# Performance work log

Hardware: AMD Instinct MI355X
Metric: run time of the kernel (lower is better)

The kernel has to match this reference:

```python
import jax, jax.numpy as jnp
import numpy as np

B, C, D, H, W = 2, 32, 16, 64, 64
SCALER = 8
CK = C // SCALER  # qk channels = 4


def setup_inputs() -> dict:
    key = jax.random.key(0)
    ks = jax.random.split(key, 8)
    s = 0.05
    return {
        "x": jax.random.normal(ks[0], (B, C, D, H, W), dtype=jnp.float32),
        "Wk": jax.random.normal(ks[1], (CK, C), dtype=jnp.float32) * s,
        "bk": jax.random.normal(ks[2], (CK,), dtype=jnp.float32) * s,
        "Wq": jax.random.normal(ks[3], (CK, C), dtype=jnp.float32) * s,
        "bq": jax.random.normal(ks[4], (CK,), dtype=jnp.float32) * s,
        "Wv": jax.random.normal(ks[5], (C, C), dtype=jnp.float32) * s,
        "bv": jax.random.normal(ks[6], (C,), dtype=jnp.float32) * s,
        "gamma": jnp.ones((1,), dtype=jnp.float32),
    }


def _proj(x, Wt, b):
    # 1x1x1 Conv3d == channel matmul: (o,c) x (b,c,d,h,w) -> (b,o,d,h,w)
    y = jnp.einsum('oc,bcdhw->bodhw', Wt, x) + b[None, :, None, None, None]
    return y


def reference(x, Wk, bk, Wq, bq, Wv, bv, gamma):
    b, c, d, h, w = x.shape
    hw = h * w
    xk = _proj(x, Wk, bk).reshape(b, -1, hw)   # (b, ck*d, hw)
    xq = _proj(x, Wq, bq).reshape(b, -1, hw)   # (b, ck*d, hw)
    xv = _proj(x, Wv, bv).reshape(b, -1, hw)   # (b, c*d,  hw)
    # dot[b,i,j] = sum_e xk[b,e,i] * xq[b,e,j]  -> (b, hw, hw)
    dot = jnp.einsum('bei,bej->bij', xk, xq)
    att = jax.nn.softmax(dot, axis=-1)          # softmax over last dim
    # x_a[b,m,i] = sum_j xv[b,m,j] * att[b,i,j]
    x_a = jnp.einsum('bmj,bij->bmi', xv, att)
    x_a = x_a.reshape(b, c, d, h, w)
    return gamma[0] * x + x_a
```

## Files before the change

kernel.cpp:

```cpp
#include <hip/hip_runtime.h>
#include <hip/hip_bf16.h>

#define B_   2
#define C_   32
#define D_   16
#define HW_  4096
#define CK_  4
#define E_   64
#define M_   512
#define JC_  4

typedef __attribute__((ext_vector_type(8)))  short bf16x8;
typedef __attribute__((ext_vector_type(16))) float f32x16;
typedef __attribute__((ext_vector_type(2)))  unsigned int u32x2;

union U4 { unsigned int u[4]; bf16x8 v; };

__device__ __forceinline__ short f2bf(float f) {
    __hip_bfloat16 h = __float2bfloat16(f);
    return *reinterpret_cast<short*>(&h);
}
__device__ __forceinline__ unsigned short f2bfu(float f) {
    __hip_bfloat16 h = __float2bfloat16(f);
    return *reinterpret_cast<unsigned short*>(&h);
}

__global__ void prep_kernel(
    const float* __restrict__ Wk, const float* __restrict__ bk,
    const float* __restrict__ Wq, const float* __restrict__ bq,
    const float* __restrict__ Wv, const float* __restrict__ bv,
    short* __restrict__ Wall, float* __restrict__ ball)
{
    int t = threadIdx.x;
    for (int i = t; i < 64*C_; i += 256) {
        int o = i >> 5, cc = i & 31;
        float val = (o < 32) ? Wv[o*C_ + cc]
                  : (o < 36) ? Wk[(o-32)*C_ + cc]
                  : (o < 40) ? Wq[(o-36)*C_ + cc] : 0.f;
        Wall[o*C_ + cc] = f2bf(val);
    }
    if (t < 64)
        ball[t] = (t < 32) ? bv[t] : (t < 36) ? bk[t-32] : (t < 40) ? bq[t-36] : 0.f;
}

__global__ __launch_bounds__(256) void proj_kernel(
    const float* __restrict__ x,
    const short* __restrict__ Wall, const float* __restrict__ ball,
    short* __restrict__ xk, short* __restrict__ xq,
    __hip_bfloat16* __restrict__ v)
{
    __shared__ short s_k[32*16], s_q[32*16];
    const int t    = threadIdx.x;
    const int lane = t & 63;
    const int w    = t >> 6;
    const int h    = lane >> 5;
    const int c    = lane & 31;

    const int pt = blockIdx.x & 127;
    const int dg = (blockIdx.x >> 7) & 3;
    const int b  = blockIdx.x >> 9;
    const int d  = dg*4 + w;
    const int p0 = pt*32;

    bf16x8 af[2][2];
    #pragma unroll
    for (int mt = 0; mt < 2; ++mt)
        #pragma unroll
        for (int s = 0; s < 2; ++s)
            af[mt][s] = *(const bf16x8*)(Wall + (mt*32 + c)*C_ + s*16 + h*8);

    U4 xb[2];
    #pragma unroll
    for (int s = 0; s < 2; ++s) {
        #pragma unroll
        for (int j = 0; j < 4; ++j) {
            int c0 = s*16 + h*8 + 2*j;
            union { float f; unsigned int u; } ua, ub;
            ua.f = x[(((size_t)(b*C_ + c0  )*D_ + d)*HW_) + p0 + c];
            ub.f = x[(((size_t)(b*C_ + c0+1)*D_ + d)*HW_) + p0 + c];
            xb[s].u[j] = __builtin_amdgcn_perm(ub.u, ua.u, 0x07060302);
        }
    }

    f32x16 a0, a1;
    #pragma unroll
    for (int r = 0; r < 16; ++r) { a0[r] = 0.f; a1[r] = 0.f; }
    #pragma unroll
    for (int s = 0; s < 2; ++s) {
        a0 = __builtin_amdgcn_mfma_f32_32x32x16_bf16(af[0][s], xb[s].v, a0, 0, 0, 0);
        a1 = __builtin_amdgcn_mfma_f32_32x32x16_bf16(af[1][s], xb[s].v, a1, 0, 0, 0);
    }

    #pragma unroll
    for (int r = 0; r < 16; ++r) {
        int o = (r & 3) + 8*(r >> 2) + 4*h;
        v[((size_t)b*M_ + (o*D_ + d))*HW_ + p0 + c] = __float2bfloat16(a0[r] + ball[o]);
    }

    #pragma unroll
    for (int r = 0; r < 4; ++r) {
        if (h == 0) s_k[c*16 + w*4 + r] = f2bf(a1[r] + ball[32 + r]);
        else        s_q[c*16 + w*4 + r] = f2bf(a1[r] + ball[36 + r]);
    }
    __syncthreads();

    const int p = t >> 3, seg = t & 7;
    size_t gb = ((size_t)b*HW_ + p0 + p)*E_ + dg*16 + seg*2;
    *(unsigned int*)(xk + gb) = *(const unsigned int*)(&s_k[p*16 + seg*2]);
    *(unsigned int*)(xq + gb) = *(const unsigned int*)(&s_q[p*16 + seg*2]);
}

__device__ __forceinline__ void load_lds16(const short* g, short* l) {
    __builtin_amdgcn_global_load_lds((const __attribute__((address_space(1))) void*)g,
                                     (__attribute__((address_space(3))) void*)l,
                                     16, 0, 0);
}

__global__ __launch_bounds__(256, 4) void attn_kernel(
    const short* __restrict__ xk_, const short* __restrict__ xq_,
    const short* __restrict__ v_,
    unsigned short* __restrict__ Op, float* __restrict__ lw)
{
    __shared__ short s_xq[2][2048];
    __shared__ short s_v [2][4096];

    const int t    = threadIdx.x;
    const int lane = t & 63;
    const int w    = t >> 6;
    const int h    = lane >> 5;
    const int c    = lane & 31;

    const int cls  = blockIdx.x & 7;
    const int b    = cls >> 2, mg = cls & 3;
    const int rest = blockIdx.x >> 3;
    const int ig   = rest & 31;
    const int jc   = rest >> 5;
    const int i0   = ig*128 + w*32;
    const int jbase = jc*(HW_/JC_);

    const short* xk_g = xk_ + (size_t)b*HW_*E_;
    const short* xq_g = xq_ + (size_t)b*HW_*E_;
    const short* v_g  = v_  + (size_t)b*M_*HW_ + (size_t)mg*128*HW_;

    bf16x8 kb[4];
    #pragma unroll
    for (int s = 0; s < 4; ++s)
        kb[s] = *(const bf16x8*)(xk_g + (size_t)(i0 + c)*E_ + s*16 + h*8);

    f32x16 acc[4];
    #pragma unroll
    for (int mt = 0; mt < 4; ++mt)
        #pragma unroll
        for (int r = 0; r < 16; ++r) acc[mt][r] = 0.f;
    float lp = 0.f;

    auto stage = [&](int buf, int j0) {
        {
            int r_ = w*8 + (lane>>3), cc = (lane&7) ^ (r_&7);
            load_lds16(xq_g + (size_t)(j0 + r_)*E_ + cc*8, &s_xq[buf][w*512]);
        }
        #pragma unroll
        for (int k = 0; k < 2; ++k) {
            int r0 = w*32 + k*16;
            int r_ = r0 + (lane>>2);
            int g  = (lane&3) ^ ((r_>>1)&3);
            load_lds16(v_g + (size_t)r_*HW_ + j0 + g*8, &s_v[buf][r0*32]);
        }
    };

    stage(0, jbase);
    __syncthreads();

    for (int it = 0; it < (HW_/JC_)/32; ++it) {
        const int cur = it & 1;
        if (it + 1 < (HW_/JC_)/32)
            stage(cur^1, jbase + (it+1)*32);

        f32x16 st;
        #pragma unroll
        for (int r = 0; r < 16; ++r) st[r] = 0.f;
        #pragma unroll
        for (int s = 0; s < 4; ++s) {
            int slot = (s*2 + h) ^ (c & 7);
            bf16x8 a1 = *(const bf16x8*)(&s_xq[cur][c*64 + slot*8]);
            st = __builtin_amdgcn_mfma_f32_32x32x16_bf16(a1, kb[s], st, 0, 0, 0);
        }

        unsigned int dq[8];
        #pragma unroll
        for (int qd = 0; qd < 8; ++qd) {
            union { float f; unsigned int u; } ua, ub;
            float e0 = __expf(st[2*qd]);
            float e1 = __expf(st[2*qd+1]);
            lp += e0 + e1;
            ua.f = e0; ub.f = e1;
            dq[qd] = __builtin_amdgcn_perm(ub.u, ua.u, 0x07060302);
        }

        U4 a2[2];
        {
            u32x2 r02 = __builtin_amdgcn_permlane32_swap(dq[0], dq[2], false, false);
            u32x2 r13 = __builtin_amdgcn_permlane32_swap(dq[1], dq[3], false, false);
            u32x2 r46 = __builtin_amdgcn_permlane32_swap(dq[4], dq[6], false, false);
            u32x2 r57 = __builtin_amdgcn_permlane32_swap(dq[5], dq[7], false, false);
            a2[0].u[0] = r02[0]; a2[0].u[1] = r13[0];
            a2[0].u[2] = r02[1]; a2[0].u[3] = r13[1];
            a2[1].u[0] = r46[0]; a2[1].u[1] = r57[0];
            a2[1].u[2] = r46[1]; a2[1].u[3] = r57[1];
        }

        #pragma unroll
        for (int s2 = 0; s2 < 2; ++s2) {
            #pragma unroll
            for (int mt = 0; mt < 4; ++mt) {
                int rowm = mt*32 + c;
                int slot = (s2*2 + h) ^ ((rowm>>1)&3);
                bf16x8 vb = *(const bf16x8*)(&s_v[cur][rowm*32 + slot*8]);
                acc[mt] = __builtin_amdgcn_mfma_f32_32x32x16_bf16(a2[s2].v, vb, acc[mt], 0, 0, 0);
            }
        }
        __syncthreads();
    }

    float l = lp + __shfl_xor(lp, 32, 64);
    if (h == 0 && mg == 0)
        lw[(size_t)(jc*B_ + b)*HW_ + i0 + c] = l;

    const size_t opb = ((size_t)(jc*B_ + b)*M_ + mg*128)*HW_;
    #pragma unroll
    for (int mt = 0; mt < 4; ++mt) {
        size_t rb = opb + (size_t)(mt*32 + c)*HW_ + i0;
        #pragma unroll
        for (int g = 0; g < 4; ++g) {
            ushort4 s4;
            s4.x = f2bfu(acc[mt][4*g+0]);
            s4.y = f2bfu(acc[mt][4*g+1]);
            s4.z = f2bfu(acc[mt][4*g+2]);
            s4.w = f2bfu(acc[mt][4*g+3]);
            *(ushort4*)(Op + rb + 8*g + 4*h) = s4;
        }
    }
}

__global__ __launch_bounds__(256) void reduce_kernel(
    const float* __restrict__ x, const float* __restrict__ gamma_p,
    const unsigned short* __restrict__ Op, const float* __restrict__ lw,
    float* __restrict__ out)
{
    size_t idx = ((size_t)blockIdx.x*256 + threadIdx.x)*4;
    int i = idx & (HW_-1);
    size_t bm = idx >> 12;
    int m = bm & (M_-1);
    int b = (int)(bm >> 9);

    float4 o = {0.f,0.f,0.f,0.f};
    float4 l = {0.f,0.f,0.f,0.f};
    #pragma unroll
    for (int jc = 0; jc < JC_; ++jc) {
        ushort4 ov = *(const ushort4*)(Op + ((size_t)(jc*B_ + b)*M_ + m)*HW_ + i);
        o.x += __uint_as_float((unsigned int)ov.x << 16);
        o.y += __uint_as_float((unsigned int)ov.y << 16);
        o.z += __uint_as_float((unsigned int)ov.z << 16);
        o.w += __uint_as_float((unsigned int)ov.w << 16);
        float4 lv = *(const float4*)(lw + (size_t)(jc*B_ + b)*HW_ + i);
        l.x += lv.x; l.y += lv.y; l.z += lv.z; l.w += lv.w;
    }
    const float gamma = gamma_p[0];
    float4 xv = *(const float4*)(x + idx);
    float4 r;
    r.x = gamma*xv.x + o.x / l.x;
    r.y = gamma*xv.y + o.y / l.y;
    r.z = gamma*xv.z + o.z / l.z;
    r.w = gamma*xv.w + o.w / l.w;
    *(float4*)(out + idx) = r;
}

extern "C" void kernel_launch(void* const* d_in, const int* in_sizes, int n_in,
                              void* d_out, int out_size, void* d_ws, size_t ws_size,
                              hipStream_t stream)
{
    const float* x     = (const float*)d_in[0];
    const float* Wk    = (const float*)d_in[1];
    const float* bk    = (const float*)d_in[2];
    const float* Wq    = (const float*)d_in[3];
    const float* bq    = (const float*)d_in[4];
    const float* Wv    = (const float*)d_in[5];
    const float* bv    = (const float*)d_in[6];
    const float* gamma = (const float*)d_in[7];
    float* out = (float*)d_out;

    char* ws = (char*)d_ws;
    short*          xk   = (short*)(ws);
    short*          xq   = (short*)(ws + (1<<20));
    short*          v    = (short*)(ws + (2<<20));
    short*          Wall = (short*)(ws + (10<<20));
    float*          ball = (float*)(ws + (10<<20) + 4096);
    unsigned short* Op   = (unsigned short*)(ws + (10<<20) + 8192);
    float*          lw   = (float*)(ws + (10<<20) + 8192
                                    + (size_t)JC_*B_*M_*HW_*2);

    prep_kernel<<<1, 256, 0, stream>>>(Wk, bk, Wq, bq, Wv, bv, Wall, ball);
    proj_kernel<<<B_*(D_/4)*(HW_/32), 256, 0, stream>>>(x, Wall, ball, xk, xq,
                                                        (__hip_bfloat16*)v);
    attn_kernel<<<8*32*JC_, 256, 0, stream>>>(xk, xq, v, Op, lw);
    reduce_kernel<<<(B_*M_*HW_)/(256*4), 256, 0, stream>>>(x, gamma, Op, lw, out);
}
```

Baseline: 162.5 us.

## Fuse weight prep into projection and split-K reduction into attention via counters

The weight-prep kernel is removed. The projection kernel now reads and converts the fp32 weights and biases itself and also zeroes a counter array. The separate reduce kernel is folded into the attention kernel: each block increments an atomic counter per (b, mg, ig) tile, and the last of the JC_ split blocks sums the partial outputs and row sums and writes the final result. s_setprio is also placed around the MFMA sections. This saves two kernel launches and a full pass over the output, but it adds fences, atomics and a serialized tail on the last-arriving block, and every mg block now writes lw redundantly.

Result: slower. 342.1 us (+110.5%).

```diff
diff --git a/kernel.cpp b/kernel.cpp
--- a/kernel.cpp
+++ b/kernel.cpp
@@ -25,29 +25,13 @@
     return *reinterpret_cast<unsigned short*>(&h);
 }
 
-__global__ void prep_kernel(
+__global__ __launch_bounds__(256) void proj_kernel(
+    const float* __restrict__ x,
     const float* __restrict__ Wk, const float* __restrict__ bk,
     const float* __restrict__ Wq, const float* __restrict__ bq,
     const float* __restrict__ Wv, const float* __restrict__ bv,
-    short* __restrict__ Wall, float* __restrict__ ball)
-{
-    int t = threadIdx.x;
-    for (int i = t; i < 64*C_; i += 256) {
-        int o = i >> 5, cc = i & 31;
-        float val = (o < 32) ? Wv[o*C_ + cc]
-                  : (o < 36) ? Wk[(o-32)*C_ + cc]
-                  : (o < 40) ? Wq[(o-36)*C_ + cc] : 0.f;
-        Wall[o*C_ + cc] = f2bf(val);
-    }
-    if (t < 64)
-        ball[t] = (t < 32) ? bv[t] : (t < 36) ? bk[t-32] : (t < 40) ? bq[t-36] : 0.f;
-}
-
-__global__ __launch_bounds__(256) void proj_kernel(
-    const float* __restrict__ x,
-    const short* __restrict__ Wall, const float* __restrict__ ball,
     short* __restrict__ xk, short* __restrict__ xq,
-    __hip_bfloat16* __restrict__ v)
+    __hip_bfloat16* __restrict__ v, unsigned int* __restrict__ cnt)
 {
     __shared__ short s_k[32*16], s_q[32*16];
     const int t    = threadIdx.x;
@@ -56,6 +40,8 @@
     const int h    = lane >> 5;
     const int c    = lane & 31;
 
+    if (blockIdx.x == 0) cnt[t] = 0;
+
     const int pt = blockIdx.x & 127;
     const int dg = (blockIdx.x >> 7) & 3;
     const int b  = blockIdx.x >> 9;
@@ -64,10 +50,15 @@
 
     bf16x8 af[2][2];
     #pragma unroll
-    for (int mt = 0; mt < 2; ++mt)
-        #pragma unroll
-        for (int s = 0; s < 2; ++s)
-            af[mt][s] = *(const bf16x8*)(Wall + (mt*32 + c)*C_ + s*16 + h*8);
+    for (int s = 0; s < 2; ++s) {
+        const float* wv = Wv + c*C_ + s*16 + h*8;
+        #pragma unroll
+        for (int k = 0; k < 8; ++k) af[0][s][k] = f2bf(wv[k]);
+        const float* wu = (c < 4) ? (Wk + c*C_ + s*16 + h*8)
+                        : (c < 8) ? (Wq + (c-4)*C_ + s*16 + h*8) : nullptr;
+        #pragma unroll
+        for (int k = 0; k < 8; ++k) af[1][s][k] = f2bf(wu ? wu[k] : 0.f);
+    }
 
     U4 xb[2];
     #pragma unroll
@@ -94,13 +85,13 @@
     #pragma unroll
     for (int r = 0; r < 16; ++r) {
         int o = (r & 3) + 8*(r >> 2) + 4*h;
-        v[((size_t)b*M_ + (o*D_ + d))*HW_ + p0 + c] = __float2bfloat16(a0[r] + ball[o]);
+        v[((size_t)b*M_ + (o*D_ + d))*HW_ + p0 + c] = __float2bfloat16(a0[r] + bv[o]);
     }
 
     #pragma unroll
     for (int r = 0; r < 4; ++r) {
-        if (h == 0) s_k[c*16 + w*4 + r] = f2bf(a1[r] + ball[32 + r]);
-        else        s_q[c*16 + w*4 + r] = f2bf(a1[r] + ball[36 + r]);
+        if (h == 0) s_k[c*16 + w*4 + r] = f2bf(a1[r] + bk[r]);
+        else        s_q[c*16 + w*4 + r] = f2bf(a1[r] + bq[r]);
     }
     __syncthreads();
 
@@ -119,10 +110,13 @@
 __global__ __launch_bounds__(256, 4) void attn_kernel(
     const short* __restrict__ xk_, const short* __restrict__ xq_,
     const short* __restrict__ v_,
-    unsigned short* __restrict__ Op, float* __restrict__ lw)
+    unsigned short* __restrict__ Op, float* __restrict__ lw,
+    const float* __restrict__ x, const float* __restrict__ gamma_p,
+    float* __restrict__ out, unsigned int* __restrict__ cnt)
 {
     __shared__ short s_xq[2][2048];
     __shared__ short s_v [2][4096];
+    __shared__ unsigned int s_old;
 
     const int t    = threadIdx.x;
     const int lane = t & 63;
@@ -179,12 +173,14 @@
         f32x16 st;
         #pragma unroll
         for (int r = 0; r < 16; ++r) st[r] = 0.f;
+        __builtin_amdgcn_s_setprio(1);
         #pragma unroll
         for (int s = 0; s < 4; ++s) {
             int slot = (s*2 + h) ^ (c & 7);
             bf16x8 a1 = *(const bf16x8*)(&s_xq[cur][c*64 + slot*8]);
             st = __builtin_amdgcn_mfma_f32_32x32x16_bf16(a1, kb[s], st, 0, 0, 0);
         }
+        __builtin_amdgcn_s_setprio(0);
 
         unsigned int dq[8];
         #pragma unroll
@@ -209,6 +205,7 @@
             a2[1].u[2] = r46[1]; a2[1].u[3] = r57[1];
         }
 
+        __builtin_amdgcn_s_setprio(1);
         #pragma unroll
         for (int s2 = 0; s2 < 2; ++s2) {
             #pragma unroll
@@ -219,11 +216,12 @@
                 acc[mt] = __builtin_amdgcn_mfma_f32_32x32x16_bf16(a2[s2].v, vb, acc[mt], 0, 0, 0);
             }
         }
+        __builtin_amdgcn_s_setprio(0);
         __syncthreads();
     }
 
     float l = lp + __shfl_xor(lp, 32, 64);
-    if (h == 0 && mg == 0)
+    if (h == 0)
         lw[(size_t)(jc*B_ + b)*HW_ + i0 + c] = l;
 
     const size_t opb = ((size_t)(jc*B_ + b)*M_ + mg*128)*HW_;
@@ -240,39 +238,42 @@
             *(ushort4*)(Op + rb + 8*g + 4*h) = s4;
         }
     }
-}
-
-__global__ __launch_bounds__(256) void reduce_kernel(
-    const float* __restrict__ x, const float* __restrict__ gamma_p,
-    const unsigned short* __restrict__ Op, const float* __restrict__ lw,
-    float* __restrict__ out)
-{
-    size_t idx = ((size_t)blockIdx.x*256 + threadIdx.x)*4;
-    int i = idx & (HW_-1);
-    size_t bm = idx >> 12;
-    int m = bm & (M_-1);
-    int b = (int)(bm >> 9);
-
-    float4 o = {0.f,0.f,0.f,0.f};
-    float4 l = {0.f,0.f,0.f,0.f};
-    #pragma unroll
-    for (int jc = 0; jc < JC_; ++jc) {
-        ushort4 ov = *(const ushort4*)(Op + ((size_t)(jc*B_ + b)*M_ + m)*HW_ + i);
-        o.x += __uint_as_float((unsigned int)ov.x << 16);
-        o.y += __uint_as_float((unsigned int)ov.y << 16);
-        o.z += __uint_as_float((unsigned int)ov.z << 16);
-        o.w += __uint_as_float((unsigned int)ov.w << 16);
-        float4 lv = *(const float4*)(lw + (size_t)(jc*B_ + b)*HW_ + i);
-        l.x += lv.x; l.y += lv.y; l.z += lv.z; l.w += lv.w;
-    }
-    const float gamma = gamma_p[0];
-    float4 xv = *(const float4*)(x + idx);
-    float4 r;
-    r.x = gamma*xv.x + o.x / l.x;
-    r.y = gamma*xv.y + o.y / l.y;
-    r.z = gamma*xv.z + o.z / l.z;
-    r.w = gamma*xv.w + o.w / l.w;
-    *(float4*)(out + idx) = r;
+
+    __threadfence();
+    if (t == 0)
+        s_old = atomicAdd(&cnt[(unsigned)((b*4 + mg)*32 + ig)], 1u);
+    __syncthreads();
+    if (s_old == JC_ - 1) {
+        __threadfence();
+        const float gamma = gamma_p[0];
+        const int mbase = mg*128, ibase = ig*128;
+        #pragma unroll 1
+        for (int k2 = 0; k2 < 16; ++k2) {
+            int e    = k2*256 + t;
+            int i    = ibase + (e & 31)*4;
+            int m    = mbase + (e >> 5);
+            float4 o4 = {0.f,0.f,0.f,0.f};
+            float4 l4 = {0.f,0.f,0.f,0.f};
+            #pragma unroll
+            for (int j2 = 0; j2 < JC_; ++j2) {
+                ushort4 ov = *(const ushort4*)(Op + ((size_t)(j2*B_ + b)*M_ + m)*HW_ + i);
+                o4.x += __uint_as_float((unsigned int)ov.x << 16);
+                o4.y += __uint_as_float((unsigned int)ov.y << 16);
+                o4.z += __uint_as_float((unsigned int)ov.z << 16);
+                o4.w += __uint_as_float((unsigned int)ov.w << 16);
+                float4 lv = *(const float4*)(lw + (size_t)(j2*B_ + b)*HW_ + i);
+                l4.x += lv.x; l4.y += lv.y; l4.z += lv.z; l4.w += lv.w;
+            }
+            size_t gidx = ((size_t)b*M_ + m)*HW_ + i;
+            float4 xv = *(const float4*)(x + gidx);
+            float4 r;
+            r.x = gamma*xv.x + o4.x / l4.x;
+            r.y = gamma*xv.y + o4.y / l4.y;
+            r.z = gamma*xv.z + o4.z / l4.z;
+            r.w = gamma*xv.w + o4.w / l4.w;
+            *(float4*)(out + gidx) = r;
+        }
+    }
 }
 
 extern "C" void kernel_launch(void* const* d_in, const int* in_sizes, int n_in,
@@ -293,15 +294,12 @@
     short*          xk   = (short*)(ws);
     short*          xq   = (short*)(ws + (1<<20));
     short*          v    = (short*)(ws + (2<<20));
-    short*          Wall = (short*)(ws + (10<<20));
-    float*          ball = (float*)(ws + (10<<20) + 4096);
+    unsigned int*   cnt  = (unsigned int*)(ws + (10<<20));
     unsigned short* Op   = (unsigned short*)(ws + (10<<20) + 8192);
     float*          lw   = (float*)(ws + (10<<20) + 8192
                                     + (size_t)JC_*B_*M_*HW_*2);
 
-    prep_kernel<<<1, 256, 0, stream>>>(Wk, bk, Wq, bq, Wv, bv, Wall, ball);
-    proj_kernel<<<B_*(D_/4)*(HW_/32), 256, 0, stream>>>(x, Wall, ball, xk, xq,
-                                                        (__hip_bfloat16*)v);
-    attn_kernel<<<8*32*JC_, 256, 0, stream>>>(xk, xq, v, Op, lw);
-    reduce_kernel<<<(B_*M_*HW_)/(256*4), 256, 0, stream>>>(x, gamma, Op, lw, out);
-}
+    proj_kernel<<<B_*(D_/4)*(HW_/32), 256, 0, stream>>>(x, Wk, bk, Wq, bq, Wv, bv,
+                                                        xk, xq, (__hip_bfloat16*)v, cnt);
+    attn_kernel<<<8*32*JC_, 256, 0, stream>>>(xk, xq, v, Op, lw, x, gamma, out, cnt);
+}
```

## Fold weight prep into projection kernel and raise wave priority around MFMA

Applied to the files above, without the earlier changes.

Removes the separate single-block prep kernel: each projection block now loads and converts the fp32 Wv/Wk/Wq rows to bf16 itself and reads the biases directly. This drops one kernel launch and its serial dependency, at the cost of redundant weight loads and conversions in every block. Separately, the attention loop wraps its two MFMA sections in s_setprio(1)/s_setprio(0) so waves issuing matrix ops get scheduling priority over waves doing exp and packing work.

After: 161.8 us. No clear change (-0.4%).

```diff
diff --git a/kernel.cpp b/kernel.cpp
--- a/kernel.cpp
+++ b/kernel.cpp
@@ -25,27 +25,11 @@
     return *reinterpret_cast<unsigned short*>(&h);
 }
 
-__global__ void prep_kernel(
+__global__ __launch_bounds__(256) void proj_kernel(
+    const float* __restrict__ x,
     const float* __restrict__ Wk, const float* __restrict__ bk,
     const float* __restrict__ Wq, const float* __restrict__ bq,
     const float* __restrict__ Wv, const float* __restrict__ bv,
-    short* __restrict__ Wall, float* __restrict__ ball)
-{
-    int t = threadIdx.x;
-    for (int i = t; i < 64*C_; i += 256) {
-        int o = i >> 5, cc = i & 31;
-        float val = (o < 32) ? Wv[o*C_ + cc]
-                  : (o < 36) ? Wk[(o-32)*C_ + cc]
-                  : (o < 40) ? Wq[(o-36)*C_ + cc] : 0.f;
-        Wall[o*C_ + cc] = f2bf(val);
-    }
-    if (t < 64)
-        ball[t] = (t < 32) ? bv[t] : (t < 36) ? bk[t-32] : (t < 40) ? bq[t-36] : 0.f;
-}
-
-__global__ __launch_bounds__(256) void proj_kernel(
-    const float* __restrict__ x,
-    const short* __restrict__ Wall, const float* __restrict__ ball,
     short* __restrict__ xk, short* __restrict__ xq,
     __hip_bfloat16* __restrict__ v)
 {
@@ -64,10 +48,15 @@
 
     bf16x8 af[2][2];
     #pragma unroll
-    for (int mt = 0; mt < 2; ++mt)
-        #pragma unroll
-        for (int s = 0; s < 2; ++s)
-            af[mt][s] = *(const bf16x8*)(Wall + (mt*32 + c)*C_ + s*16 + h*8);
+    for (int s = 0; s < 2; ++s) {
+        const float* wv = Wv + c*C_ + s*16 + h*8;
+        #pragma unroll
+        for (int k = 0; k < 8; ++k) af[0][s][k] = f2bf(wv[k]);
+        const float* wu = (c < 4) ? (Wk + c*C_ + s*16 + h*8)
+                        : (c < 8) ? (Wq + (c-4)*C_ + s*16 + h*8) : nullptr;
+        #pragma unroll
+        for (int k = 0; k < 8; ++k) af[1][s][k] = f2bf(wu ? wu[k] : 0.f);
+    }
 
     U4 xb[2];
     #pragma unroll
@@ -94,13 +83,13 @@
     #pragma unroll
     for (int r = 0; r < 16; ++r) {
         int o = (r & 3) + 8*(r >> 2) + 4*h;
-        v[((size_t)b*M_ + (o*D_ + d))*HW_ + p0 + c] = __float2bfloat16(a0[r] + ball[o]);
+        v[((size_t)b*M_ + (o*D_ + d))*HW_ + p0 + c] = __float2bfloat16(a0[r] + bv[o]);
     }
 
     #pragma unroll
     for (int r = 0; r < 4; ++r) {
-        if (h == 0) s_k[c*16 + w*4 + r] = f2bf(a1[r] + ball[32 + r]);
-        else        s_q[c*16 + w*4 + r] = f2bf(a1[r] + ball[36 + r]);
+        if (h == 0) s_k[c*16 + w*4 + r] = f2bf(a1[r] + bk[r]);
+        else        s_q[c*16 + w*4 + r] = f2bf(a1[r] + bq[r]);
     }
     __syncthreads();
 
@@ -179,12 +168,14 @@
         f32x16 st;
         #pragma unroll
         for (int r = 0; r < 16; ++r) st[r] = 0.f;
+        __builtin_amdgcn_s_setprio(1);
         #pragma unroll
         for (int s = 0; s < 4; ++s) {
             int slot = (s*2 + h) ^ (c & 7);
             bf16x8 a1 = *(const bf16x8*)(&s_xq[cur][c*64 + slot*8]);
             st = __builtin_amdgcn_mfma_f32_32x32x16_bf16(a1, kb[s], st, 0, 0, 0);
         }
+        __builtin_amdgcn_s_setprio(0);
 
         unsigned int dq[8];
         #pragma unroll
@@ -209,6 +200,7 @@
             a2[1].u[2] = r46[1]; a2[1].u[3] = r57[1];
         }
 
+        __builtin_amdgcn_s_setprio(1);
         #pragma unroll
         for (int s2 = 0; s2 < 2; ++s2) {
             #pragma unroll
@@ -219,6 +211,7 @@
                 acc[mt] = __builtin_amdgcn_mfma_f32_32x32x16_bf16(a2[s2].v, vb, acc[mt], 0, 0, 0);
             }
         }
+        __builtin_amdgcn_s_setprio(0);
         __syncthreads();
     }
 
@@ -293,15 +286,12 @@
     short*          xk   = (short*)(ws);
     short*          xq   = (short*)(ws + (1<<20));
     short*          v    = (short*)(ws + (2<<20));
-    short*          Wall = (short*)(ws + (10<<20));
-    float*          ball = (float*)(ws + (10<<20) + 4096);
     unsigned short* Op   = (unsigned short*)(ws + (10<<20) + 8192);
     float*          lw   = (float*)(ws + (10<<20) + 8192
                                     + (size_t)JC_*B_*M_*HW_*2);
 
-    prep_kernel<<<1, 256, 0, stream>>>(Wk, bk, Wq, bq, Wv, bv, Wall, ball);
-    proj_kernel<<<B_*(D_/4)*(HW_/32), 256, 0, stream>>>(x, Wall, ball, xk, xq,
-                                                        (__hip_bfloat16*)v);
+    proj_kernel<<<B_*(D_/4)*(HW_/32), 256, 0, stream>>>(x, Wk, bk, Wq, bq, Wv, bv,
+                                                        xk, xq, (__hip_bfloat16*)v);
     attn_kernel<<<8*32*JC_, 256, 0, stream>>>(xk, xq, v, Op, lw);
     reduce_kernel<<<(B_*M_*HW_)/(256*4), 256, 0, stream>>>(x, gamma, Op, lw, out);
 }
```
